# Kernel tuning notes

Hardware: AMD Instinct MI355X
Metric: run time of the kernel (lower is better)

## Reference

```python
import jax, jax.numpy as jnp
import numpy as np

N, P, Q, H_DIM, HEADS, D = 4096, 128, 128, 256, 8, 64  # D = graph_dim // heads


def setup_inputs() -> dict:
    key = jax.random.key(0)
    ks = jax.random.split(key, 6)
    s = 0.05  # small scale to keep tanh/softmax in a sane range
    return {
        "x_prices": jax.random.normal(ks[0], (N, P), jnp.float32),
        "x_news": jax.random.normal(ks[1], (N, Q), jnp.float32),
        "W_bil": jax.random.normal(ks[2], (H_DIM, P, Q), jnp.float32) * s,
        "b_bil": jax.random.normal(ks[3], (H_DIM,), jnp.float32) * s,
        "Wt": jax.random.normal(ks[4], (HEADS, D, H_DIM), jnp.float32) * s,
        "a_vec": jax.random.normal(ks[5], (HEADS, 2 * D), jnp.float32) * s,
    }


def reference(x_prices, x_news, W_bil, b_bil, Wt, a_vec):
    # nn.Bilinear: out[n,h] = sum_pq x_prices[n,p] W[h,p,q] x_news[n,q] + b[h]
    x = jnp.einsum('np,hpq,nq->nh', x_prices, W_bil, x_news) + b_bil  # (N, hidden)

    # Per-head linear transform: fc_transform (no bias). Wt: (heads, d, hidden)
    xt = jnp.einsum('nh,kdh->knd', x, Wt)  # (heads, N, d)

    # Attention score a . [x_i, x_j] split into src/dst halves -> broadcast add
    d = Wt.shape[1]
    a_src, a_dst = a_vec[:, :d], a_vec[:, d:]
    s_src = jnp.einsum('knd,kd->kn', xt, a_src)  # (heads, N)
    s_dst = jnp.einsum('knd,kd->kn', xt, a_dst)  # (heads, N)
    scores = s_src[:, :, None] + s_dst[:, None, :]  # (heads, N, N)
    scores = jnp.where(scores >= 0, scores, 0.2 * scores)  # LeakyReLU(0.2)

    attn = jax.nn.softmax(scores, axis=-1)  # softmax over neighbors j
    out = jnp.einsum('knm,kmd->knd', attn, xt)  # (heads, N, d)

    # Concatenate head outputs on feature dim, then tanh
    out = jnp.transpose(out, (1, 0, 2)).reshape(xt.shape[1], -1)  # (N, heads*d)
    return jnp.tanh(out)
```

## Files before the change

### kernel.cpp

```cpp
#include <hip/hip_runtime.h>
#include <hip/hip_bf16.h>

typedef unsigned short ushort;
typedef unsigned int uint;
typedef unsigned long long u64;
typedef _Float16 f16;

#define NN 4096
#define PP 128
#define QQ 128
#define HD 256
#define KH 8
#define DD 64
#define KK 16384

typedef _Float16 f16x2 __attribute__((ext_vector_type(2)));
typedef _Float16 f16x4 __attribute__((ext_vector_type(4)));
typedef _Float16 f16x8 __attribute__((ext_vector_type(8)));
typedef __fp16 fp16x2 __attribute__((ext_vector_type(2)));
typedef float f32x4 __attribute__((ext_vector_type(4)));

__device__ inline void async_lds16(const void* g, void* l) {
  __builtin_amdgcn_global_load_lds(
      (const __attribute__((address_space(1))) unsigned int*)g,
      (__attribute__((address_space(3))) unsigned int*)l, 16, 0, 0);
}

__global__ __launch_bounds__(256) void k0_split2(
    const float* __restrict__ W, const float* __restrict__ Wt,
    f16* __restrict__ hiW, f16* __restrict__ loW,
    f16* __restrict__ hiT, f16* __restrict__ loT, float* __restrict__ xz) {
  const int tid = blockIdx.x * 256 + threadIdx.x;
  const int i = tid * 4;
  if (tid < (NN * HD) / 4)
    *(float4*)&xz[i] = make_float4(0.f, 0.f, 0.f, 0.f);
  const float* src;
  f16 *hi, *lo;
  int off;
  if (i < HD * PP * QQ) { src = W; hi = hiW; lo = loW; off = i; }
  else { src = Wt; hi = hiT; lo = loT; off = i - HD * PP * QQ; }
  const float4 w = *(const float4*)&src[off];
  const float wf[4] = {w.x, w.y, w.z, w.w};
  f16x4 hv, lv;
#pragma unroll
  for (int j = 0; j < 4; ++j) {
    const f16 h = (f16)wf[j];
    hv[j] = h;
    lv[j] = (f16)(wf[j] - (float)h);
  }
  *(f16x4*)&hi[off] = hv;
  *(f16x4*)&lo[off] = lv;
}

__global__ __launch_bounds__(256, 4) void k1_bilinear(
    const float* __restrict__ xp, const float* __restrict__ xn,
    const f16* __restrict__ Whi, const f16* __restrict__ Wlo,
    float* __restrict__ xout) {
  __shared__ f16 whi[128 * 32];
  __shared__ f16 wlo[128 * 32];
  __shared__ f16 zhi[128 * 32];
  __shared__ float xpt[8][128];

  const int t = threadIdx.x;
  const int bid = blockIdx.x;
  const int xcd = bid & 7, slot = bid >> 3;
  const int jpan = slot >> 5, n_idx = slot & 31;
  const int pan = xcd + 8 * jpan;
  const int n0 = n_idx * 128;
  const int kb = (pan & 15) * (KK / 16);
  const int h0 = (pan >> 4) * 128;
  const int pb = kb >> 7;

  for (int idx = t; idx < 1024; idx += 256) {
    const int p = idx & 7, n = idx >> 3;
    xpt[p][n] = xp[(size_t)(n0 + n) * PP + pb + p];
  }

  const int l = t & 63, w = t >> 6;
  const int wr = (w >> 1) * 64, wc = (w & 1) * 64;

  int aoff[4], boff[4];
#pragma unroll
  for (int i = 0; i < 4; ++i) {
    const int row = wr + i * 16 + (l & 15);
    aoff[i] = row * 32 + (((l >> 4) ^ ((row ^ (row >> 2)) & 3)) * 8);
  }
#pragma unroll
  for (int j = 0; j < 4; ++j) {
    const int hr = wc + j * 16 + (l & 15);
    boff[j] = hr * 32 + (((l >> 4) ^ ((hr ^ (hr >> 2)) & 3)) * 8);
  }

  const int shb = t >> 2, seg = t & 3;
  int gsw[2];
#pragma unroll
  for (int g = 0; g < 2; ++g) {
    const int r = shb + 64 * g;
    gsw[g] = seg ^ ((r ^ (r >> 2)) & 3);
  }

  const int zn = t >> 1, zko = (t & 1) * 16;
  const int zm = (zn ^ (zn >> 2)) & 3;
  const int zs0 = (t & 1) * 2;
  const int zo0 = zn * 32 + ((zs0 ^ zm) * 8);
  const int zo1 = zn * 32 + (((zs0 + 1) ^ zm) * 8);

  f32x4 acc[4][4];
#pragma unroll
  for (int i = 0; i < 4; ++i)
#pragma unroll
    for (int j = 0; j < 4; ++j) acc[i][j] = (f32x4)0.f;

  const float* xr0 = xn + (size_t)(n0 + zn) * QQ + zko;
  float4 xv0 = ((const float4*)xr0)[0];
  float4 xv1 = ((const float4*)xr0)[1];
  float4 xv2 = ((const float4*)xr0)[2];
  float4 xv3 = ((const float4*)xr0)[3];

  for (int c = 0; c < 32; ++c) {
    const int kc = kb + c * 32;
    const int pl = c >> 2;

    __syncthreads();

#pragma unroll
    for (int g = 0; g < 2; ++g) {
      const int r = shb + 64 * g;
      async_lds16(Whi + (size_t)(h0 + r) * KK + kc + gsw[g] * 8,
                  whi + r * 32 + seg * 8);
      async_lds16(Wlo + (size_t)(h0 + r) * KK + kc + gsw[g] * 8,
                  wlo + r * 32 + seg * 8);
    }

    {
      const float xpv = xpt[pl][zn];
      float zz[16] = {xv0.x, xv0.y, xv0.z, xv0.w, xv1.x, xv1.y, xv1.z, xv1.w,
                      xv2.x, xv2.y, xv2.z, xv2.w, xv3.x, xv3.y, xv3.z, xv3.w};
      union { uint u[8]; uint4 q[2]; } ph;
#pragma unroll
      for (int j = 0; j < 8; ++j) {
        union { fp16x2 h; uint u; } cv;
        cv.h = __builtin_amdgcn_cvt_pkrtz(xpv * zz[2 * j], xpv * zz[2 * j + 1]);
        ph.u[j] = cv.u;
      }
      *(uint4*)&zhi[zo0] = ph.q[0];
      *(uint4*)&zhi[zo1] = ph.q[1];
    }

    __syncthreads();

    if (c < 31) {
      const int q0n = ((c + 1) & 3) * 32;
      const float* xr = xn + (size_t)(n0 + zn) * QQ + q0n + zko;
      xv0 = ((const float4*)xr)[0];
      xv1 = ((const float4*)xr)[1];
      xv2 = ((const float4*)xr)[2];
      xv3 = ((const float4*)xr)[3];
    }

    f16x8 Ah[4];
#pragma unroll
    for (int i = 0; i < 4; ++i) Ah[i] = *(const f16x8*)&zhi[aoff[i]];
#pragma unroll
    for (int j = 0; j < 4; ++j) {
      const f16x8 Bh = *(const f16x8*)&whi[boff[j]];
      const f16x8 Bl = *(const f16x8*)&wlo[boff[j]];
#pragma unroll
      for (int i = 0; i < 4; ++i)
        acc[i][j] = __builtin_amdgcn_mfma_f32_16x16x32_f16(Ah[i], Bh, acc[i][j], 0, 0, 0);
#pragma unroll
      for (int i = 0; i < 4; ++i)
        acc[i][j] = __builtin_amdgcn_mfma_f32_16x16x32_f16(Ah[i], Bl, acc[i][j], 0, 0, 0);
    }
  }

#pragma unroll
  for (int i = 0; i < 4; ++i)
#pragma unroll
    for (int j = 0; j < 4; ++j) {
      const int row = n0 + wr + i * 16 + (l >> 4) * 4;
      const int col = h0 + wc + j * 16 + (l & 15);
#pragma unroll
      for (int r = 0; r < 4; ++r)
        atomicAdd(&xout[(size_t)(row + r) * HD + col], acc[i][j][r]);
    }
}

__global__ __launch_bounds__(256) void k23_xt(
    const float* __restrict__ x, const float* __restrict__ bb,
    const f16* __restrict__ Wthi, const f16* __restrict__ Wtlo,
    const float* __restrict__ av, float* __restrict__ xt,
    float* __restrict__ ssrc, float* __restrict__ sdst) {
  __shared__ f16 ah[64 * 32];
  __shared__ f16 bh[128 * 32];
  __shared__ f16 bl[128 * 32];
  __shared__ float red1[2][64][17];
  __shared__ float red2[2][64][17];
  const int t = threadIdx.x;
  const int n0 = blockIdx.x * 64;
  const int c0 = blockIdx.y * 128;
  const int l = t & 63, w = t >> 6;
  const int wn = (w & 1) * 32, wcc = (w >> 1) * 64;

  int aoff[2], boff[4];
#pragma unroll
  for (int i = 0; i < 2; ++i) {
    const int row = wn + i * 16 + (l & 15);
    aoff[i] = row * 32 + (((l >> 4) ^ ((row ^ (row >> 2)) & 3)) * 8);
  }
#pragma unroll
  for (int j = 0; j < 4; ++j) {
    const int hr = wcc + j * 16 + (l & 15);
    boff[j] = hr * 32 + (((l >> 4) ^ ((hr ^ (hr >> 2)) & 3)) * 8);
  }

  f32x4 acc[2][4];
#pragma unroll
  for (int i = 0; i < 2; ++i)
#pragma unroll
    for (int j = 0; j < 4; ++j) acc[i][j] = (f32x4)0.f;

  for (int kc = 0; kc < HD; kc += 32) {
    __syncthreads();
    {
      const int row = t >> 2, sg = t & 3;
      const float* xr = &x[(size_t)(n0 + row) * HD + kc + sg * 8];
      const float4 xa = ((const float4*)xr)[0];
      const float4 xb = ((const float4*)xr)[1];
      const float4 ba = *(const float4*)&bb[kc + sg * 8];
      const float4 bv = *(const float4*)&bb[kc + sg * 8 + 4];
      f16x8 o;
      o[0] = (f16)(xa.x + ba.x); o[1] = (f16)(xa.y + ba.y);
      o[2] = (f16)(xa.z + ba.z); o[3] = (f16)(xa.w + ba.w);
      o[4] = (f16)(xb.x + bv.x); o[5] = (f16)(xb.y + bv.y);
      o[6] = (f16)(xb.z + bv.z); o[7] = (f16)(xb.w + bv.w);
      const int sgs = sg ^ ((row ^ (row >> 2)) & 3);
      *(f16x8*)&ah[row * 32 + sgs * 8] = o;
    }
#pragma unroll
    for (int g = 0; g < 2; ++g) {
      const int slot = g * 256 + t;
      const int col = slot >> 2, ps = slot & 3;
      const int ls = ps ^ ((col ^ (col >> 2)) & 3);
      *(uint4*)&bh[col * 32 + ps * 8] =
          *(const uint4*)&Wthi[(size_t)(c0 + col) * HD + kc + ls * 8];
      *(uint4*)&bl[col * 32 + ps * 8] =
          *(const uint4*)&Wtlo[(size_t)(c0 + col) * HD + kc + ls * 8];
    }
    __syncthreads();
    f16x8 Af[2];
#pragma unroll
    for (int i = 0; i < 2; ++i) Af[i] = *(const f16x8*)&ah[aoff[i]];
#pragma unroll
    for (int j = 0; j < 4; ++j) {
      const f16x8 Bh = *(const f16x8*)&bh[boff[j]];
      const f16x8 Bl = *(const f16x8*)&bl[boff[j]];
#pragma unroll
      for (int i = 0; i < 2; ++i)
        acc[i][j] = __builtin_amdgcn_mfma_f32_16x16x32_f16(Af[i], Bh, acc[i][j], 0, 0, 0);
#pragma unroll
      for (int i = 0; i < 2; ++i)
        acc[i][j] = __builtin_amdgcn_mfma_f32_16x16x32_f16(Af[i], Bl, acc[i][j], 0, 0, 0);
    }
  }

  const int hh = w >> 1;
  const int khead = (c0 >> 6) + hh;
  float a1v[4], a2v[4];
#pragma unroll
  for (int j = 0; j < 4; ++j) {
    const int d = j * 16 + (l & 15);
    a1v[j] = av[khead * (2 * DD) + d];
    a2v[j] = av[khead * (2 * DD) + DD + d];
  }

#pragma unroll
  for (int i = 0; i < 2; ++i)
#pragma unroll
    for (int r = 0; r < 4; ++r) {
      const int rowl = wn + i * 16 + (l >> 4) * 4 + r;
      float p1 = 0.f, p2 = 0.f;
#pragma unroll
      for (int j = 0; j < 4; ++j) {
        p1 += acc[i][j][r] * a1v[j];
        p2 += acc[i][j][r] * a2v[j];
      }
      red1[hh][rowl][l & 15] = p1;
      red2[hh][rowl][l & 15] = p2;
    }

#pragma unroll
  for (int i = 0; i < 2; ++i)
#pragma unroll
    for (int j = 0; j < 4; ++j) {
      const int row = n0 + wn + i * 16 + (l >> 4) * 4;
      const int colg = c0 + wcc + j * 16 + (l & 15);
      const int k = colg >> 6, d = colg & 63;
#pragma unroll
      for (int r = 0; r < 4; ++r)
        xt[((size_t)(k * NN + row + r)) * DD + d] = acc[i][j][r];
    }

  __syncthreads();
  {
    const int hh2 = t >> 7;
    const int which = (t >> 6) & 1;
    const int row = t & 63;
    const float* rp = which ? &red2[hh2][row][0] : &red1[hh2][row][0];
    float s = 0.f;
#pragma unroll
    for (int g = 0; g < 16; ++g) s += rp[g];
    const int kk = (c0 >> 6) + hh2;
    if (which) sdst[kk * NN + n0 + row] = s;
    else ssrc[kk * NN + n0 + row] = s;
  }
}

__global__ __launch_bounds__(256) void k4_rank(
    const float* __restrict__ sdst, float* __restrict__ vsorted,
    int* __restrict__ perm) {
  __shared__ u64 kv[4096];
  __shared__ ushort pcnt[256];
  const int k = blockIdx.y, t = threadIdx.x;
  for (int i = t; i < 4096; i += 256) {
    const uint u = __float_as_uint(sdst[k * NN + i]);
    const uint key = (u & 0x80000000u) ? ~u : (u | 0x80000000u);
    kv[i] = ((u64)key << 32) | (uint)i;
  }
  __syncthreads();
  const int idx = t & 127;
  const int half = t >> 7;
  const u64 my = kv[blockIdx.x * 128 + idx];
  const int j0 = half * 2048;
  int cnt = 0;
#pragma unroll 16
  for (int j = 0; j < 2048; ++j) cnt += (kv[j0 + j] < my) ? 1 : 0;
  pcnt[t] = (ushort)cnt;
  __syncthreads();
  if (t < 128) {
    const int tot = (int)pcnt[t] + (int)pcnt[t + 128];
    const u64 my2 = kv[blockIdx.x * 128 + t];
    const uint key = (uint)(my2 >> 32);
    const uint u = (key & 0x80000000u) ? (key ^ 0x80000000u) : ~key;
    vsorted[k * NN + tot] = __uint_as_float(u);
    perm[k * NN + tot] = (int)(my2 & 0xFFFFFFFFu);
  }
}

__global__ __launch_bounds__(64) void k4b_chunksum(
    const float* __restrict__ vs, const int* __restrict__ perm,
    const float* __restrict__ xt, float* __restrict__ Chi, float* __restrict__ Clo) {
  __shared__ float rows[64][64];
  __shared__ float eh[64], el[64];
  const int c = blockIdx.x, k = blockIdx.y, t = threadIdx.x;
  const int base = k * NN + c * 64;
  {
    const float v = vs[base + t];
    eh[t] = __expf(v);
    el[t] = __expf(0.2f * v);
  }
#pragma unroll
  for (int r = 0; r < 16; ++r) {
    const int i = r * 4 + (t >> 4);
    const int p = perm[base + i];
    *(float4*)&rows[i][(t & 15) * 4] =
        *(const float4*)&xt[((size_t)(k * NN + p)) * DD + (t & 15) * 4];
  }
  __syncthreads();
  float shi = 0.f, slo = 0.f, whs = 0.f, wls = 0.f;
#pragma unroll 8
  for (int i = 0; i < 64; ++i) {
    const float val = rows[i][t];
    shi += eh[i] * val; slo += el[i] * val;
    whs += eh[i]; wls += el[i];
  }
  const int cb = (k * 64 + c) * 65;
  Chi[cb + t] = shi;
  Clo[cb + t] = slo;
  if (t == 0) { Chi[cb + 64] = whs; Clo[cb + 64] = wls; }
}

__global__ __launch_bounds__(64) void k4d_expand(
    const float* __restrict__ vs, const int* __restrict__ perm,
    const float* __restrict__ xt, const float* __restrict__ Chi,
    const float* __restrict__ Clo, float* __restrict__ Phi,
    float* __restrict__ Plo) {
  __shared__ float scs[64 * 65];
  __shared__ float rows[64][64];
  __shared__ float ev[64];
  const int c = blockIdx.x, k = blockIdx.y, t = threadIdx.x;
  const int pass = blockIdx.z;
  const int base = k * NN + c * 64;
  const float* Cs = pass ? Chi : Clo;
  for (int idx = t; idx < 4160; idx += 64) scs[idx] = Cs[k * 4160 + idx];
  {
    const float v = vs[base + t];
    ev[t] = pass ? __expf(v) : __expf(0.2f * v);
  }
#pragma unroll
  for (int r = 0; r < 16; ++r) {
    const int i = r * 4 + (t >> 4);
    const int p = perm[base + i];
    *(float4*)&rows[i][(t & 15) * 4] =
        *(const float4*)&xt[((size_t)(k * NN + p)) * DD + (t & 15) * 4];
  }
  __syncthreads();

  if (pass == 0) {
    float run = 0.f, wrun = 0.f;
    for (int cc = 0; cc < c; ++cc) {
      run += scs[cc * 65 + t];
      wrun += scs[cc * 65 + 64];
    }
    for (int i = 0; i < 64; ++i) {
      const size_t rb = ((size_t)(k * 4097) + c * 64 + i) * 65;
      Plo[rb + t] = run;
      if (t == 0) Plo[rb + 64] = wrun;
      run += ev[i] * rows[i][t];
      wrun += ev[i];
    }
    if (c == 63) {
      const size_t rb = ((size_t)(k * 4097) + 4096) * 65;
      Plo[rb + t] = run;
      if (t == 0) Plo[rb + 64] = wrun;
    }
  } else {
    float runS = 0.f, wrunS = 0.f;
    for (int cc = c + 1; cc < 64; ++cc) {
      runS += scs[cc * 65 + t];
      wrunS += scs[cc * 65 + 64];
    }
    for (int i = 63; i >= 0; --i) {
      runS += ev[i] * rows[i][t];
      wrunS += ev[i];
      const size_t rb = ((size_t)(k * 4097) + c * 64 + i) * 65;
      Phi[rb + t] = runS;
      if (t == 0) Phi[rb + 64] = wrunS;
    }
    if (c == 63) {
      const size_t rb = ((size_t)(k * 4097) + 4096) * 65;
      Phi[rb + t] = 0.f;
      if (t == 0) Phi[rb + 64] = 0.f;
    }
  }
}

__global__ __launch_bounds__(256) void k6_final(
    const float* __restrict__ ssrc, const float* __restrict__ vsorted,
    const float* __restrict__ Phi, const float* __restrict__ Plo,
    float* __restrict__ out) {
  __shared__ float vsh[4096];
  __shared__ int posSh[16];
  const int t = threadIdx.x;
  const int q0 = blockIdx.x * 16;
  const int k = q0 >> 12;
  for (int idx = t; idx < 1024; idx += 256)
    *(float4*)&vsh[idx * 4] = *(const float4*)&vsorted[k * NN + idx * 4];
  __syncthreads();
  if (t < 16) {
    const float thr = -ssrc[q0 + t];
    int lo = 0, hi = 4096;
    while (lo < hi) {
      const int mid = (lo + hi) >> 1;
      if (vsh[mid] < thr) lo = mid + 1; else hi = mid;
    }
    posSh[t] = lo;
  }
  __syncthreads();
  const int d = t & 63;
#pragma unroll
  for (int qq = 0; qq < 4; ++qq) {
    const int ql = qq * 4 + (t >> 6);
    const int qi = q0 + ql;
    const int n = qi & 4095;
    const float u = ssrc[qi];
    const size_t rb = ((size_t)(k * 4097) + posSh[ql]) * 65;
    const float eu = __expf(u), el = __expf(0.2f * u);
    const float num = eu * Phi[rb + d] + el * Plo[rb + d];
    const float den = eu * Phi[rb + 64] + el * Plo[rb + 64];
    out[(size_t)n * (KH * DD) + k * DD + d] = tanhf(num / den);
  }
}

extern "C" void kernel_launch(void* const* d_in, const int* in_sizes, int n_in,
                              void* d_out, int out_size, void* d_ws, size_t ws_size,
                              hipStream_t stream) {
  const float* xp = (const float*)d_in[0];
  const float* xn = (const float*)d_in[1];
  const float* W = (const float*)d_in[2];
  const float* bb = (const float*)d_in[3];
  const float* Wt = (const float*)d_in[4];
  const float* av = (const float*)d_in[5];
  float* out = (float*)d_out;

  char* ws = (char*)d_ws;
  f16* Whi    = (f16*)(ws);
  f16* Wlo    = (f16*)(ws + 8388608);
  float* Phi  = (float*)(ws);
  float* Plo  = (float*)(ws + 8522240);
  float* x    = (float*)(ws + 17044480);
  float* xt   = (float*)(ws + 21238784);
  f16* Wthi   = (f16*)(ws + 31724544);
  f16* Wtlo   = (f16*)(ws + 31986688);
  float* ssrc = (float*)(ws + 32248832);
  float* sdst = (float*)(ws + 32379904);
  float* vsort= (float*)(ws + 32510976);
  int*   perm = (int*)  (ws + 32642048);
  float* Chi  = (float*)(ws + 32773120);
  float* Clo  = (float*)(ws + 32906240);

  k0_split2<<<(HD * PP * QQ + KH * DD * HD) / 1024, 256, 0, stream>>>(
      W, Wt, Whi, Wlo, Wthi, Wtlo, x);
  k1_bilinear<<<1024, 256, 0, stream>>>(xp, xn, Whi, Wlo, x);
  k23_xt<<<dim3(NN / 64, 4), 256, 0, stream>>>(x, bb, Wthi, Wtlo, av, xt, ssrc, sdst);
  k4_rank<<<dim3(32, KH), 256, 0, stream>>>(sdst, vsort, perm);
  k4b_chunksum<<<dim3(64, KH), 64, 0, stream>>>(vsort, perm, xt, Chi, Clo);
  k4d_expand<<<dim3(64, KH, 2), 64, 0, stream>>>(vsort, perm, xt, Chi, Clo, Phi, Plo);
  k6_final<<<(KH * NN) / 16, 256, 0, stream>>>(ssrc, vsort, Phi, Plo, out);
}
```

Measured before the change: 246.7 us.

## Retile bilinear GEMM to 128x64 output tiles with 64-wide K chunks

The bilinear kernel's block tile changes from 128 rows x 128 hidden to 128 rows x 64 hidden, and each K step grows from 32 to 64 with two MFMA sub-steps per barrier pair. The grid doubles to 2048 blocks, and the LDS swizzle is redone for 64-wide rows. The aim is to halve the number of barrier-synchronised chunks and give more blocks for occupancy. In exchange, the xnews-derived A operand is rebuilt twice as often relative to the hidden dimension, and the atomic output traffic layout changes.

```diff
diff --git a/kernel.cpp b/kernel.cpp
--- a/kernel.cpp
+++ b/kernel.cpp
@@ -56,9 +56,9 @@
     const float* __restrict__ xp, const float* __restrict__ xn,
     const f16* __restrict__ Whi, const f16* __restrict__ Wlo,
     float* __restrict__ xout) {
-  __shared__ f16 whi[128 * 32];
-  __shared__ f16 wlo[128 * 32];
-  __shared__ f16 zhi[128 * 32];
+  __shared__ f16 whi[64 * 64];
+  __shared__ f16 wlo[64 * 64];
+  __shared__ f16 zhi[128 * 64];
   __shared__ float xpt[8][128];
 
   const int t = threadIdx.x;
@@ -67,8 +67,8 @@
   const int jpan = slot >> 5, n_idx = slot & 31;
   const int pan = xcd + 8 * jpan;
   const int n0 = n_idx * 128;
-  const int kb = (pan & 15) * (KK / 16);
-  const int h0 = (pan >> 4) * 128;
+  const int kb = (pan & 15) * 1024;
+  const int h0 = (pan >> 4) * 64;
   const int pb = kb >> 7;
 
   for (int idx = t; idx < 1024; idx += 256) {
@@ -77,109 +77,109 @@
   }
 
   const int l = t & 63, w = t >> 6;
-  const int wr = (w >> 1) * 64, wc = (w & 1) * 64;
-
-  int aoff[4], boff[4];
+  const int wn = (w & 1) * 64, wh = (w >> 1) * 32;
+
+  int aoff[4][2], boff[2][2];
 #pragma unroll
   for (int i = 0; i < 4; ++i) {
-    const int row = wr + i * 16 + (l & 15);
-    aoff[i] = row * 32 + (((l >> 4) ^ ((row ^ (row >> 2)) & 3)) * 8);
-  }
-#pragma unroll
-  for (int j = 0; j < 4; ++j) {
-    const int hr = wc + j * 16 + (l & 15);
-    boff[j] = hr * 32 + (((l >> 4) ^ ((hr ^ (hr >> 2)) & 3)) * 8);
-  }
-
-  const int shb = t >> 2, seg = t & 3;
-  int gsw[2];
-#pragma unroll
-  for (int g = 0; g < 2; ++g) {
-    const int r = shb + 64 * g;
-    gsw[g] = seg ^ ((r ^ (r >> 2)) & 3);
-  }
-
-  const int zn = t >> 1, zko = (t & 1) * 16;
-  const int zm = (zn ^ (zn >> 2)) & 3;
-  const int zs0 = (t & 1) * 2;
-  const int zo0 = zn * 32 + ((zs0 ^ zm) * 8);
-  const int zo1 = zn * 32 + (((zs0 + 1) ^ zm) * 8);
-
-  f32x4 acc[4][4];
+    const int row = wn + i * 16 + (l & 15);
+#pragma unroll
+    for (int ks = 0; ks < 2; ++ks)
+      aoff[i][ks] = row * 64 + (((ks * 4 + (l >> 4)) ^ (row & 7)) * 8);
+  }
+#pragma unroll
+  for (int j = 0; j < 2; ++j) {
+    const int hr = wh + j * 16 + (l & 15);
+#pragma unroll
+    for (int ks = 0; ks < 2; ++ks)
+      boff[j][ks] = hr * 64 + (((ks * 4 + (l >> 4)) ^ (hr & 7)) * 8);
+  }
+
+  const int swrow = t >> 3, swseg = t & 7;
+  const int sgsw = swseg ^ (swrow & 7);
+
+  const int zn = t >> 1, zko = (t & 1) * 32;
+  const int zsegbase = zko >> 3;
+  const int zm = zn & 7;
+
+  f32x4 acc[4][2];
 #pragma unroll
   for (int i = 0; i < 4; ++i)
 #pragma unroll
-    for (int j = 0; j < 4; ++j) acc[i][j] = (f32x4)0.f;
-
-  const float* xr0 = xn + (size_t)(n0 + zn) * QQ + zko;
-  float4 xv0 = ((const float4*)xr0)[0];
-  float4 xv1 = ((const float4*)xr0)[1];
-  float4 xv2 = ((const float4*)xr0)[2];
-  float4 xv3 = ((const float4*)xr0)[3];
-
-  for (int c = 0; c < 32; ++c) {
-    const int kc = kb + c * 32;
-    const int pl = c >> 2;
+    for (int j = 0; j < 2; ++j) acc[i][j] = (f32x4)0.f;
+
+  float4 xv[8];
+  {
+    const float* xr = xn + (size_t)(n0 + zn) * QQ + zko;
+#pragma unroll
+    for (int u = 0; u < 8; ++u) xv[u] = ((const float4*)xr)[u];
+  }
+
+  for (int c = 0; c < 16; ++c) {
+    const int kc = kb + c * 64;
+    const int pl = c >> 1;
 
     __syncthreads();
 
 #pragma unroll
     for (int g = 0; g < 2; ++g) {
-      const int r = shb + 64 * g;
-      async_lds16(Whi + (size_t)(h0 + r) * KK + kc + gsw[g] * 8,
-                  whi + r * 32 + seg * 8);
-      async_lds16(Wlo + (size_t)(h0 + r) * KK + kc + gsw[g] * 8,
-                  wlo + r * 32 + seg * 8);
+      const int r = swrow + 32 * g;
+      async_lds16(Whi + (size_t)(h0 + r) * KK + kc + sgsw * 8,
+                  whi + r * 64 + swseg * 8);
+      async_lds16(Wlo + (size_t)(h0 + r) * KK + kc + sgsw * 8,
+                  wlo + r * 64 + swseg * 8);
     }
 
     {
       const float xpv = xpt[pl][zn];
-      float zz[16] = {xv0.x, xv0.y, xv0.z, xv0.w, xv1.x, xv1.y, xv1.z, xv1.w,
-                      xv2.x, xv2.y, xv2.z, xv2.w, xv3.x, xv3.y, xv3.z, xv3.w};
-      union { uint u[8]; uint4 q[2]; } ph;
-#pragma unroll
-      for (int j = 0; j < 8; ++j) {
-        union { fp16x2 h; uint u; } cv;
-        cv.h = __builtin_amdgcn_cvt_pkrtz(xpv * zz[2 * j], xpv * zz[2 * j + 1]);
-        ph.u[j] = cv.u;
+      union { uint u[16]; uint4 q[4]; } ph;
+#pragma unroll
+      for (int u = 0; u < 8; ++u) {
+        union { fp16x2 h; uint uu; } c0, c1;
+        c0.h = __builtin_amdgcn_cvt_pkrtz(xpv * xv[u].x, xpv * xv[u].y);
+        c1.h = __builtin_amdgcn_cvt_pkrtz(xpv * xv[u].z, xpv * xv[u].w);
+        ph.u[2 * u] = c0.uu;
+        ph.u[2 * u + 1] = c1.uu;
       }
-      *(uint4*)&zhi[zo0] = ph.q[0];
-      *(uint4*)&zhi[zo1] = ph.q[1];
+#pragma unroll
+      for (int s = 0; s < 4; ++s)
+        *(uint4*)&zhi[zn * 64 + ((zsegbase + s) ^ zm) * 8] = ph.q[s];
     }
 
     __syncthreads();
 
-    if (c < 31) {
-      const int q0n = ((c + 1) & 3) * 32;
+    if (c < 15) {
+      const int q0n = ((c + 1) & 1) * 64;
       const float* xr = xn + (size_t)(n0 + zn) * QQ + q0n + zko;
-      xv0 = ((const float4*)xr)[0];
-      xv1 = ((const float4*)xr)[1];
-      xv2 = ((const float4*)xr)[2];
-      xv3 = ((const float4*)xr)[3];
-    }
-
-    f16x8 Ah[4];
-#pragma unroll
-    for (int i = 0; i < 4; ++i) Ah[i] = *(const f16x8*)&zhi[aoff[i]];
-#pragma unroll
-    for (int j = 0; j < 4; ++j) {
-      const f16x8 Bh = *(const f16x8*)&whi[boff[j]];
-      const f16x8 Bl = *(const f16x8*)&wlo[boff[j]];
-#pragma unroll
-      for (int i = 0; i < 4; ++i)
-        acc[i][j] = __builtin_amdgcn_mfma_f32_16x16x32_f16(Ah[i], Bh, acc[i][j], 0, 0, 0);
-#pragma unroll
-      for (int i = 0; i < 4; ++i)
-        acc[i][j] = __builtin_amdgcn_mfma_f32_16x16x32_f16(Ah[i], Bl, acc[i][j], 0, 0, 0);
+#pragma unroll
+      for (int u = 0; u < 8; ++u) xv[u] = ((const float4*)xr)[u];
+    }
+
+#pragma unroll
+    for (int ks = 0; ks < 2; ++ks) {
+      f16x8 Ah[4];
+#pragma unroll
+      for (int i = 0; i < 4; ++i) Ah[i] = *(const f16x8*)&zhi[aoff[i][ks]];
+#pragma unroll
+      for (int j = 0; j < 2; ++j) {
+        const f16x8 Bh = *(const f16x8*)&whi[boff[j][ks]];
+        const f16x8 Bl = *(const f16x8*)&wlo[boff[j][ks]];
+#pragma unroll
+        for (int i = 0; i < 4; ++i)
+          acc[i][j] = __builtin_amdgcn_mfma_f32_16x16x32_f16(Ah[i], Bh, acc[i][j], 0, 0, 0);
+#pragma unroll
+        for (int i = 0; i < 4; ++i)
+          acc[i][j] = __builtin_amdgcn_mfma_f32_16x16x32_f16(Ah[i], Bl, acc[i][j], 0, 0, 0);
+      }
     }
   }
 
 #pragma unroll
   for (int i = 0; i < 4; ++i)
 #pragma unroll
-    for (int j = 0; j < 4; ++j) {
-      const int row = n0 + wr + i * 16 + (l >> 4) * 4;
-      const int col = h0 + wc + j * 16 + (l & 15);
+    for (int j = 0; j < 2; ++j) {
+      const int row = n0 + wn + i * 16 + (l >> 4) * 4;
+      const int col = h0 + wh + j * 16 + (l & 15);
 #pragma unroll
       for (int r = 0; r < 4; ++r)
         atomicAdd(&xout[(size_t)(row + r) * HD + col], acc[i][j][r]);
@@ -511,7 +511,7 @@
 
   k0_split2<<<(HD * PP * QQ + KH * DD * HD) / 1024, 256, 0, stream>>>(
       W, Wt, Whi, Wlo, Wthi, Wtlo, x);
-  k1_bilinear<<<1024, 256, 0, stream>>>(xp, xn, Whi, Wlo, x);
+  k1_bilinear<<<2048, 256, 0, stream>>>(xp, xn, Whi, Wlo, x);
   k23_xt<<<dim3(NN / 64, 4), 256, 0, stream>>>(x, bb, Wthi, Wtlo, av, xt, ssrc, sdst);
   k4_rank<<<dim3(32, KH), 256, 0, stream>>>(sdst, vsort, perm);
   k4b_chunksum<<<dim3(64, KH), 64, 0, stream>>>(vsort, perm, xt, Chi, Clo);
```

New measurement: 300.0 us. 1.22x slower.

## Double-buffer bilinear W tiles and build A fragments in registers

Applied to the files above, without the earlier changes.

Restructures the bilinear kernel so each warp owns 32 rows by all 128 columns. The A operand (xp*xn products) is now built directly in registers instead of being staged through an LDS tile. The W hi/lo tiles are double-buffered, so the next chunk is loaded asynchronously while the current one feeds the MFMAs, and the two barriers per iteration become one. The cost is more LDS for the two buffers, more accumulator registers per warp, and a hand-written waitcnt whose correctness depends on vmcnt ordering.

```diff
diff --git a/kernel.cpp b/kernel.cpp
--- a/kernel.cpp
+++ b/kernel.cpp
@@ -56,9 +56,8 @@
     const float* __restrict__ xp, const float* __restrict__ xn,
     const f16* __restrict__ Whi, const f16* __restrict__ Wlo,
     float* __restrict__ xout) {
-  __shared__ f16 whi[128 * 32];
-  __shared__ f16 wlo[128 * 32];
-  __shared__ f16 zhi[128 * 32];
+  __shared__ f16 whi[2][128 * 32];
+  __shared__ f16 wlo[2][128 * 32];
   __shared__ float xpt[8][128];
 
   const int t = threadIdx.x;
@@ -71,115 +70,113 @@
   const int h0 = (pan >> 4) * 128;
   const int pb = kb >> 7;
 
+  const int l = t & 63, w = t >> 6;
+  const int rbase = w * 32 + (l & 15);
+  const int kofs = (l >> 4) * 8;
+
+  int boff[8];
+#pragma unroll
+  for (int j = 0; j < 8; ++j) {
+    const int hr = j * 16 + (l & 15);
+    boff[j] = hr * 32 + (((l >> 4) ^ ((hr ^ (hr >> 2)) & 3)) * 8);
+  }
+
+  const int shb = t >> 2, seg = t & 3;
+  int gsw[2];
+#pragma unroll
+  for (int g = 0; g < 2; ++g) {
+    const int r = shb + 64 * g;
+    gsw[g] = seg ^ ((r ^ (r >> 2)) & 3);
+  }
+
+  auto stage_w = [&](int buf, int kc_) {
+#pragma unroll
+    for (int g = 0; g < 2; ++g) {
+      const int r = shb + 64 * g;
+      async_lds16(Whi + (size_t)(h0 + r) * KK + kc_ + gsw[g] * 8,
+                  &whi[buf][r * 32 + seg * 8]);
+      async_lds16(Wlo + (size_t)(h0 + r) * KK + kc_ + gsw[g] * 8,
+                  &wlo[buf][r * 32 + seg * 8]);
+    }
+  };
+
+  const float* xrow0 = xn + (size_t)(n0 + rbase) * QQ + kofs;
+  const float* xrow1 = xrow0 + (size_t)16 * QQ;
+
+  f32x4 acc[2][8];
+#pragma unroll
+  for (int i = 0; i < 2; ++i)
+#pragma unroll
+    for (int j = 0; j < 8; ++j) acc[i][j] = (f32x4)0.f;
+
   for (int idx = t; idx < 1024; idx += 256) {
     const int p = idx & 7, n = idx >> 3;
     xpt[p][n] = xp[(size_t)(n0 + n) * PP + pb + p];
   }
-
-  const int l = t & 63, w = t >> 6;
-  const int wr = (w >> 1) * 64, wc = (w & 1) * 64;
-
-  int aoff[4], boff[4];
-#pragma unroll
-  for (int i = 0; i < 4; ++i) {
-    const int row = wr + i * 16 + (l & 15);
-    aoff[i] = row * 32 + (((l >> 4) ^ ((row ^ (row >> 2)) & 3)) * 8);
-  }
-#pragma unroll
-  for (int j = 0; j < 4; ++j) {
-    const int hr = wc + j * 16 + (l & 15);
-    boff[j] = hr * 32 + (((l >> 4) ^ ((hr ^ (hr >> 2)) & 3)) * 8);
-  }
-
-  const int shb = t >> 2, seg = t & 3;
-  int gsw[2];
-#pragma unroll
-  for (int g = 0; g < 2; ++g) {
-    const int r = shb + 64 * g;
-    gsw[g] = seg ^ ((r ^ (r >> 2)) & 3);
-  }
-
-  const int zn = t >> 1, zko = (t & 1) * 16;
-  const int zm = (zn ^ (zn >> 2)) & 3;
-  const int zs0 = (t & 1) * 2;
-  const int zo0 = zn * 32 + ((zs0 ^ zm) * 8);
-  const int zo1 = zn * 32 + (((zs0 + 1) ^ zm) * 8);
-
-  f32x4 acc[4][4];
-#pragma unroll
-  for (int i = 0; i < 4; ++i)
-#pragma unroll
-    for (int j = 0; j < 4; ++j) acc[i][j] = (f32x4)0.f;
-
-  const float* xr0 = xn + (size_t)(n0 + zn) * QQ + zko;
-  float4 xv0 = ((const float4*)xr0)[0];
-  float4 xv1 = ((const float4*)xr0)[1];
-  float4 xv2 = ((const float4*)xr0)[2];
-  float4 xv3 = ((const float4*)xr0)[3];
+  f32x4 xnP[4];
+  xnP[0] = *(const f32x4*)(xrow0);
+  xnP[1] = *(const f32x4*)(xrow0 + 4);
+  xnP[2] = *(const f32x4*)(xrow1);
+  xnP[3] = *(const f32x4*)(xrow1 + 4);
+  stage_w(0, kb);
+  __syncthreads();
+
+  float xpv0 = 0.f, xpv1 = 0.f;
 
   for (int c = 0; c < 32; ++c) {
-    const int kc = kb + c * 32;
-    const int pl = c >> 2;
-
-    __syncthreads();
-
-#pragma unroll
-    for (int g = 0; g < 2; ++g) {
-      const int r = shb + 64 * g;
-      async_lds16(Whi + (size_t)(h0 + r) * KK + kc + gsw[g] * 8,
-                  whi + r * 32 + seg * 8);
-      async_lds16(Wlo + (size_t)(h0 + r) * KK + kc + gsw[g] * 8,
-                  wlo + r * 32 + seg * 8);
-    }
-
+    const int cur = c & 1;
+    if ((c & 3) == 0) {
+      xpv0 = xpt[c >> 2][rbase];
+      xpv1 = xpt[c >> 2][rbase + 16];
+    }
+
+    f16x8 Af0, Af1;
     {
-      const float xpv = xpt[pl][zn];
-      float zz[16] = {xv0.x, xv0.y, xv0.z, xv0.w, xv1.x, xv1.y, xv1.z, xv1.w,
-                      xv2.x, xv2.y, xv2.z, xv2.w, xv3.x, xv3.y, xv3.z, xv3.w};
-      union { uint u[8]; uint4 q[2]; } ph;
-#pragma unroll
-      for (int j = 0; j < 8; ++j) {
-        union { fp16x2 h; uint u; } cv;
-        cv.h = __builtin_amdgcn_cvt_pkrtz(xpv * zz[2 * j], xpv * zz[2 * j + 1]);
-        ph.u[j] = cv.u;
-      }
-      *(uint4*)&zhi[zo0] = ph.q[0];
-      *(uint4*)&zhi[zo1] = ph.q[1];
-    }
-
-    __syncthreads();
+      union { uint u[4]; f16x8 f; } pk;
+      union { fp16x2 h; uint uu; } cv;
+      cv.h = __builtin_amdgcn_cvt_pkrtz(xpv0 * xnP[0][0], xpv0 * xnP[0][1]); pk.u[0] = cv.uu;
+      cv.h = __builtin_amdgcn_cvt_pkrtz(xpv0 * xnP[0][2], xpv0 * xnP[0][3]); pk.u[1] = cv.uu;
+      cv.h = __builtin_amdgcn_cvt_pkrtz(xpv0 * xnP[1][0], xpv0 * xnP[1][1]); pk.u[2] = cv.uu;
+      cv.h = __builtin_amdgcn_cvt_pkrtz(xpv0 * xnP[1][2], xpv0 * xnP[1][3]); pk.u[3] = cv.uu;
+      Af0 = pk.f;
+      cv.h = __builtin_amdgcn_cvt_pkrtz(xpv1 * xnP[2][0], xpv1 * xnP[2][1]); pk.u[0] = cv.uu;
+      cv.h = __builtin_amdgcn_cvt_pkrtz(xpv1 * xnP[2][2], xpv1 * xnP[2][3]); pk.u[1] = cv.uu;
+      cv.h = __builtin_amdgcn_cvt_pkrtz(xpv1 * xnP[3][0], xpv1 * xnP[3][1]); pk.u[2] = cv.uu;
+      cv.h = __builtin_amdgcn_cvt_pkrtz(xpv1 * xnP[3][2], xpv1 * xnP[3][3]); pk.u[3] = cv.uu;
+      Af1 = pk.f;
+    }
+
+    if (c < 31) stage_w(cur ^ 1, kb + (c + 1) * 32);
+
+#pragma unroll
+    for (int j = 0; j < 8; ++j) {
+      const f16x8 Bh = *(const f16x8*)&whi[cur][boff[j]];
+      const f16x8 Bl = *(const f16x8*)&wlo[cur][boff[j]];
+      acc[0][j] = __builtin_amdgcn_mfma_f32_16x16x32_f16(Af0, Bh, acc[0][j], 0, 0, 0);
+      acc[1][j] = __builtin_amdgcn_mfma_f32_16x16x32_f16(Af1, Bh, acc[1][j], 0, 0, 0);
+      acc[0][j] = __builtin_amdgcn_mfma_f32_16x16x32_f16(Af0, Bl, acc[0][j], 0, 0, 0);
+      acc[1][j] = __builtin_amdgcn_mfma_f32_16x16x32_f16(Af1, Bl, acc[1][j], 0, 0, 0);
+    }
 
     if (c < 31) {
-      const int q0n = ((c + 1) & 3) * 32;
-      const float* xr = xn + (size_t)(n0 + zn) * QQ + q0n + zko;
-      xv0 = ((const float4*)xr)[0];
-      xv1 = ((const float4*)xr)[1];
-      xv2 = ((const float4*)xr)[2];
-      xv3 = ((const float4*)xr)[3];
-    }
-
-    f16x8 Ah[4];
-#pragma unroll
-    for (int i = 0; i < 4; ++i) Ah[i] = *(const f16x8*)&zhi[aoff[i]];
-#pragma unroll
-    for (int j = 0; j < 4; ++j) {
-      const f16x8 Bh = *(const f16x8*)&whi[boff[j]];
-      const f16x8 Bl = *(const f16x8*)&wlo[boff[j]];
-#pragma unroll
-      for (int i = 0; i < 4; ++i)
-        acc[i][j] = __builtin_amdgcn_mfma_f32_16x16x32_f16(Ah[i], Bh, acc[i][j], 0, 0, 0);
-#pragma unroll
-      for (int i = 0; i < 4; ++i)
-        acc[i][j] = __builtin_amdgcn_mfma_f32_16x16x32_f16(Ah[i], Bl, acc[i][j], 0, 0, 0);
-    }
-  }
-
-#pragma unroll
-  for (int i = 0; i < 4; ++i)
-#pragma unroll
-    for (int j = 0; j < 4; ++j) {
-      const int row = n0 + wr + i * 16 + (l >> 4) * 4;
-      const int col = h0 + wc + j * 16 + (l & 15);
+      const int qn = ((c + 1) & 3) * 32;
+      xnP[0] = *(const f32x4*)(xrow0 + qn);
+      xnP[1] = *(const f32x4*)(xrow0 + qn + 4);
+      xnP[2] = *(const f32x4*)(xrow1 + qn);
+      xnP[3] = *(const f32x4*)(xrow1 + qn + 4);
+      asm volatile("s_waitcnt vmcnt(4) lgkmcnt(0)" ::: "memory");
+      __builtin_amdgcn_sched_barrier(0);
+      __builtin_amdgcn_s_barrier();
+      __builtin_amdgcn_sched_barrier(0);
+    }
+  }
+
+#pragma unroll
+  for (int i = 0; i < 2; ++i)
+#pragma unroll
+    for (int j = 0; j < 8; ++j) {
+      const int row = n0 + w * 32 + i * 16 + (l >> 4) * 4;
+      const int col = h0 + j * 16 + (l & 15);
 #pragma unroll
       for (int r = 0; r < 4; ++r)
         atomicAdd(&xout[(size_t)(row + r) * HD + col], acc[i][j][r]);
```

New measurement: 274.3 us. +11.2%, slower.

## Double-buffer bilinear weight tiles in LDS and keep x_prices in registers

Applied to the files above, without the earlier changes.

The bilinear kernel now keeps two LDS buffers for the hi/lo weight tiles and issues the async global-to-LDS load for the next chunk before building the current z tile. The goal is to hide weight load latency behind MFMA work. The shared xpt table is removed; each thread loads its 8 x_prices values straight into registers. The change doubles weight LDS use, which may lower occupancy at launch bounds of 4, and uses manual barriers with lgkmcnt waits that must correctly cover the async LDS loads.

```diff
diff --git a/kernel.cpp b/kernel.cpp
--- a/kernel.cpp
+++ b/kernel.cpp
@@ -56,10 +56,9 @@
     const float* __restrict__ xp, const float* __restrict__ xn,
     const f16* __restrict__ Whi, const f16* __restrict__ Wlo,
     float* __restrict__ xout) {
-  __shared__ f16 whi[128 * 32];
-  __shared__ f16 wlo[128 * 32];
+  __shared__ f16 whi[2][128 * 32];
+  __shared__ f16 wlo[2][128 * 32];
   __shared__ f16 zhi[128 * 32];
-  __shared__ float xpt[8][128];
 
   const int t = threadIdx.x;
   const int bid = blockIdx.x;
@@ -71,11 +70,6 @@
   const int h0 = (pan >> 4) * 128;
   const int pb = kb >> 7;
 
-  for (int idx = t; idx < 1024; idx += 256) {
-    const int p = idx & 7, n = idx >> 3;
-    xpt[p][n] = xp[(size_t)(n0 + n) * PP + pb + p];
-  }
-
   const int l = t & 63, w = t >> 6;
   const int wr = (w >> 1) * 64, wc = (w & 1) * 64;
 
@@ -98,6 +92,17 @@
     const int r = shb + 64 * g;
     gsw[g] = seg ^ ((r ^ (r >> 2)) & 3);
   }
+
+  auto stage_w = [&](int buf, int kc_) {
+#pragma unroll
+    for (int g = 0; g < 2; ++g) {
+      const int r = shb + 64 * g;
+      async_lds16(Whi + (size_t)(h0 + r) * KK + kc_ + gsw[g] * 8,
+                  &whi[buf][r * 32 + seg * 8]);
+      async_lds16(Wlo + (size_t)(h0 + r) * KK + kc_ + gsw[g] * 8,
+                  &wlo[buf][r * 32 + seg * 8]);
+    }
+  };
 
   const int zn = t >> 1, zko = (t & 1) * 16;
   const int zm = (zn ^ (zn >> 2)) & 3;
@@ -111,66 +116,79 @@
 #pragma unroll
     for (int j = 0; j < 4; ++j) acc[i][j] = (f32x4)0.f;
 
-  const float* xr0 = xn + (size_t)(n0 + zn) * QQ + zko;
-  float4 xv0 = ((const float4*)xr0)[0];
-  float4 xv1 = ((const float4*)xr0)[1];
-  float4 xv2 = ((const float4*)xr0)[2];
-  float4 xv3 = ((const float4*)xr0)[3];
-
-  for (int c = 0; c < 32; ++c) {
-    const int kc = kb + c * 32;
-    const int pl = c >> 2;
-
-    __syncthreads();
-
-#pragma unroll
-    for (int g = 0; g < 2; ++g) {
-      const int r = shb + 64 * g;
-      async_lds16(Whi + (size_t)(h0 + r) * KK + kc + gsw[g] * 8,
-                  whi + r * 32 + seg * 8);
-      async_lds16(Wlo + (size_t)(h0 + r) * KK + kc + gsw[g] * 8,
-                  wlo + r * 32 + seg * 8);
-    }
-
-    {
-      const float xpv = xpt[pl][zn];
-      float zz[16] = {xv0.x, xv0.y, xv0.z, xv0.w, xv1.x, xv1.y, xv1.z, xv1.w,
-                      xv2.x, xv2.y, xv2.z, xv2.w, xv3.x, xv3.y, xv3.z, xv3.w};
-      union { uint u[8]; uint4 q[2]; } ph;
-#pragma unroll
-      for (int j = 0; j < 8; ++j) {
-        union { fp16x2 h; uint u; } cv;
-        cv.h = __builtin_amdgcn_cvt_pkrtz(xpv * zz[2 * j], xpv * zz[2 * j + 1]);
-        ph.u[j] = cv.u;
+  float xpp[8];
+  {
+    const float* xpr = xp + (size_t)(n0 + zn) * PP + pb;
+    const f32x4 a = *(const f32x4*)xpr;
+    const f32x4 b = *(const f32x4*)(xpr + 4);
+    xpp[0] = a[0]; xpp[1] = a[1]; xpp[2] = a[2]; xpp[3] = a[3];
+    xpp[4] = b[0]; xpp[5] = b[1]; xpp[6] = b[2]; xpp[7] = b[3];
+  }
+  const float* xrow = xn + (size_t)(n0 + zn) * QQ + zko;
+  float4 xv0 = ((const float4*)xrow)[0];
+  float4 xv1 = ((const float4*)xrow)[1];
+  float4 xv2 = ((const float4*)xrow)[2];
+  float4 xv3 = ((const float4*)xrow)[3];
+  stage_w(0, kb);
+  __syncthreads();
+
+#pragma unroll
+  for (int pl = 0; pl < 8; ++pl) {
+#pragma unroll 1
+    for (int q = 0; q < 4; ++q) {
+      const int c = pl * 4 + q;
+      const int cur = c & 1;
+      const bool more = (pl < 7) || (q < 3);
+
+      asm volatile("s_waitcnt lgkmcnt(0)" ::: "memory");
+      __builtin_amdgcn_sched_barrier(0);
+      __builtin_amdgcn_s_barrier();
+      __builtin_amdgcn_sched_barrier(0);
+
+      if (more) stage_w(cur ^ 1, kb + (c + 1) * 32);
+
+      {
+        const float xpv = xpp[pl];
+        float zz[16] = {xv0.x, xv0.y, xv0.z, xv0.w, xv1.x, xv1.y, xv1.z, xv1.w,
+                        xv2.x, xv2.y, xv2.z, xv2.w, xv3.x, xv3.y, xv3.z, xv3.w};
+        union { uint u[8]; uint4 qd[2]; } ph;
+#pragma unroll
+        for (int j = 0; j < 8; ++j) {
+          union { fp16x2 h; uint u; } cv;
+          cv.h = __builtin_amdgcn_cvt_pkrtz(xpv * zz[2 * j], xpv * zz[2 * j + 1]);
+          ph.u[j] = cv.u;
+        }
+        *(uint4*)&zhi[zo0] = ph.qd[0];
+        *(uint4*)&zhi[zo1] = ph.qd[1];
       }
-      *(uint4*)&zhi[zo0] = ph.q[0];
-      *(uint4*)&zhi[zo1] = ph.q[1];
-    }
-
-    __syncthreads();
-
-    if (c < 31) {
-      const int q0n = ((c + 1) & 3) * 32;
-      const float* xr = xn + (size_t)(n0 + zn) * QQ + q0n + zko;
-      xv0 = ((const float4*)xr)[0];
-      xv1 = ((const float4*)xr)[1];
-      xv2 = ((const float4*)xr)[2];
-      xv3 = ((const float4*)xr)[3];
-    }
-
-    f16x8 Ah[4];
-#pragma unroll
-    for (int i = 0; i < 4; ++i) Ah[i] = *(const f16x8*)&zhi[aoff[i]];
-#pragma unroll
-    for (int j = 0; j < 4; ++j) {
-      const f16x8 Bh = *(const f16x8*)&whi[boff[j]];
-      const f16x8 Bl = *(const f16x8*)&wlo[boff[j]];
-#pragma unroll
-      for (int i = 0; i < 4; ++i)
-        acc[i][j] = __builtin_amdgcn_mfma_f32_16x16x32_f16(Ah[i], Bh, acc[i][j], 0, 0, 0);
-#pragma unroll
-      for (int i = 0; i < 4; ++i)
-        acc[i][j] = __builtin_amdgcn_mfma_f32_16x16x32_f16(Ah[i], Bl, acc[i][j], 0, 0, 0);
+
+      asm volatile("s_waitcnt lgkmcnt(0)" ::: "memory");
+      __builtin_amdgcn_sched_barrier(0);
+      __builtin_amdgcn_s_barrier();
+      __builtin_amdgcn_sched_barrier(0);
+
+      if (more) {
+        const int qn = ((c + 1) & 3) * 32;
+        xv0 = ((const float4*)(xrow + qn))[0];
+        xv1 = ((const float4*)(xrow + qn))[1];
+        xv2 = ((const float4*)(xrow + qn))[2];
+        xv3 = ((const float4*)(xrow + qn))[3];
+      }
+
+      f16x8 Ah[4];
+#pragma unroll
+      for (int i = 0; i < 4; ++i) Ah[i] = *(const f16x8*)&zhi[aoff[i]];
+#pragma unroll
+      for (int j = 0; j < 4; ++j) {
+        const f16x8 Bh = *(const f16x8*)&whi[cur][boff[j]];
+        const f16x8 Bl = *(const f16x8*)&wlo[cur][boff[j]];
+#pragma unroll
+        for (int i = 0; i < 4; ++i)
+          acc[i][j] = __builtin_amdgcn_mfma_f32_16x16x32_f16(Ah[i], Bh, acc[i][j], 0, 0, 0);
+#pragma unroll
+        for (int i = 0; i < 4; ++i)
+          acc[i][j] = __builtin_amdgcn_mfma_f32_16x16x32_f16(Ah[i], Bl, acc[i][j], 0, 0, 0);
+      }
     }
   }
 
```

Result: no change. 243.8 us (-1.2%).
